# Kernel tuning notes

Hardware: AMD Instinct MI355X
Metric: run time of the kernel (lower is better)

## Reference

```python
import jax, jax.numpy as jnp
import numpy as np
import math

B, NRES, RPR = 1, 384, 3
L = NRES * RPR          # 1152 rigids
CS, CZ = 256, 128
CH, H, PQ, PV = 16, 8, 8, 12


def _ln(x, scale, bias):
    mu = jnp.mean(x, axis=-1, keepdims=True)
    var = jnp.var(x, axis=-1, keepdims=True)
    return (x - mu) * jax.lax.rsqrt(var + 1e-5) * scale + bias


def _quat_to_rot(q):
    q = q / jnp.linalg.norm(q, axis=-1, keepdims=True)
    w, x, y, z = q[..., 0], q[..., 1], q[..., 2], q[..., 3]
    r = jnp.stack([
        1 - 2 * (y * y + z * z), 2 * (x * y - w * z), 2 * (x * z + w * y),
        2 * (x * y + w * z), 1 - 2 * (x * x + z * z), 2 * (y * z - w * x),
        2 * (x * z - w * y), 2 * (y * z + w * x), 1 - 2 * (x * x + y * y),
    ], axis=-1)
    return r.reshape(q.shape[:-1] + (3, 3))


def setup_inputs() -> dict:
    key = jax.random.key(0)
    ks = jax.random.split(key, 20)
    s = jax.random.normal(ks[0], (B, L, CS), jnp.float32)
    z = jax.random.normal(ks[1], (B, NRES, NRES, CZ), jnp.float32)
    rot = _quat_to_rot(jax.random.normal(ks[2], (B, L, 4), jnp.float32))
    trans = 10.0 * jax.random.normal(ks[3], (B, L, 3), jnp.float32)
    mask = jnp.ones((B, L), jnp.float32)
    rigid_to_res_idx = jnp.broadcast_to(jnp.arange(L, dtype=jnp.int32) // RPR, (B, L))
    w = lambda k, sh: 0.02 * jax.random.normal(k, sh, jnp.float32)
    return {
        "s": s, "z": z, "rot": rot, "trans": trans, "mask": mask,
        "ln_s_scale": jnp.ones((CS,), jnp.float32), "ln_s_bias": jnp.zeros((CS,), jnp.float32),
        "ln_z_scale": jnp.ones((CZ,), jnp.float32), "ln_z_bias": jnp.zeros((CZ,), jnp.float32),
        "w_q": w(ks[4], (CS, H * CH)), "w_k": w(ks[5], (CS, H * CH)), "w_v": w(ks[6], (CS, H * CH)),
        "w_qp": w(ks[7], (CS, H * PQ * 3)), "w_kp": w(ks[8], (CS, H * PQ * 3)), "w_vp": w(ks[9], (CS, H * PV * 3)),
        "w_b": w(ks[10], (CZ, H)),
        "head_weights": jnp.full((H,), 0.5413, jnp.float32),  # softplus^-1(1)
        "w_out": w(ks[11], (H * (CH + CZ + PV * 4), CS)),
        "b_out": jnp.zeros((CS,), jnp.float32),
        "rigid_to_res_idx": rigid_to_res_idx,
    }


def reference(s, z, rot, trans, mask, ln_s_scale, ln_s_bias, ln_z_scale, ln_z_bias,
              w_q, w_k, w_v, w_qp, w_kp, w_vp, w_b, head_weights, w_out, b_out,
              rigid_to_res_idx):
    b_, l_ = s.shape[0], s.shape[1]
    idx = rigid_to_res_idx[0]                       # [L] rigid -> residue, shared over batch
    s_ln = _ln(s, ln_s_scale, ln_s_bias)            # [B,L,CS]
    z_ln = _ln(z, ln_z_scale, ln_z_bias)            # [B,N,N,CZ]

    q = (s_ln @ w_q).reshape(b_, l_, H, CH)
    k = (s_ln @ w_k).reshape(b_, l_, H, CH)
    v = (s_ln @ w_v).reshape(b_, l_, H, CH)

    # local points, then rigid-transform to global frame: x_g = R x + t
    q_p = (s_ln @ w_qp).reshape(b_, l_, H, PQ, 3)
    k_p = (s_ln @ w_kp).reshape(b_, l_, H, PQ, 3)
    v_p = (s_ln @ w_vp).reshape(b_, l_, H, PV, 3)
    t5 = trans[:, :, None, None, :]
    q_g = jnp.einsum("blij,blhpj->blhpi", rot, q_p) + t5
    k_g = jnp.einsum("blij,blhpj->blhpi", rot, k_p) + t5
    v_g = jnp.einsum("blij,blhpj->blhpi", rot, v_p) + t5

    # scalar qk term
    a = jnp.einsum("blhc,bjhc->bhlj", q, k) * math.sqrt(1.0 / (3 * CH))
    # pair bias, broadcast residue-pair -> rigid-pair
    b_res = z_ln @ w_b                                # [B,N,N,H]
    b_full = b_res[:, idx][:, :, idx]                 # [B,L,L,H]
    a = a + math.sqrt(1.0 / 3) * jnp.transpose(b_full, (0, 3, 1, 2))
    # point-distance term: ||q-k||^2 = |q|^2 + |k|^2 - 2 q.k (summed over P,3)
    hw = jax.nn.softplus(head_weights) * math.sqrt(1.0 / (3 * (PQ * 9.0 / 2)))
    qq = jnp.sum(q_g * q_g, axis=(-1, -2)).transpose(0, 2, 1)   # [B,H,L]
    kk = jnp.sum(k_g * k_g, axis=(-1, -2)).transpose(0, 2, 1)
    qk = jnp.einsum("blhpc,bjhpc->bhlj", q_g, k_g)
    d2 = qq[:, :, :, None] + kk[:, :, None, :] - 2.0 * qk
    a = a - 0.5 * d2 * hw[None, :, None, None]
    a = a + (mask[:, None, None, :] - 1.0) * 1e9
    attn = jax.nn.softmax(a, axis=-1)                 # [B,H,L,L]

    o = jnp.einsum("bhlj,bjhc->blhc", attn, v)        # [B,L,H,CH]
    o_pt_g = jnp.einsum("bhlj,bjhpc->blhpc", attn, v_g)
    # back to local frame of query rigid: R^T (x - t)
    o_pt = jnp.einsum("blji,blhpj->blhpi", rot, o_pt_g - t5)
    o_pt_norm = jnp.sqrt(jnp.sum(o_pt * o_pt, axis=-1) + 1e-8)  # [B,L,H,PV]
    # pair output: sum attention over rigids belonging to each key residue
    attn_res = attn.reshape(b_, H, l_, NRES, RPR).sum(-1)       # [B,H,L,N]
    z_l = z_ln[:, idx]                                           # [B,L,N,CZ]
    o_pair = jnp.einsum("bhln,blnc->blhc", attn_res, z_l)        # [B,L,H,CZ]

    cat = jnp.concatenate(
        [o, o_pt.reshape(b_, l_, H, PV * 3), o_pt_norm, o_pair], axis=-1
    ).reshape(b_, l_, H * (CH + PV * 4 + CZ))
    return cat @ w_out + b_out                        # [B,L,CS]
```

## Files before the change

kernel.cpp:

```cpp
#include <hip/hip_runtime.h>
#include <hip/hip_bf16.h>

#define L 1152
#define NRES 384
#define CS 256
#define CZ 128
#define H 8
#define CH 16
#define PQ 8
#define PV 12
#define PSTR 1088

#define OFF_SLN  0L
#define OFF_PROJ 294912L
#define OFF_WPK  1548288L
#define OFF_QCAT 1826816L
#define OFF_KCAT 2232320L
#define OFF_VCAT 2637824L
#define OFF_BRES 3227648L
#define OFF_MURS 4407296L
#define OFF_ATTN 4702208L
#define OFF_CAT  15319040L
#define OFF_PAV  18286592L
#define OFF_POP  21825536L
#define OFF_ARES 26544128L
#define OFF_PCAT 30083072L
#define OFF_RST  32442368L

__global__ __launch_bounds__(256) void k_pre(
    const float* wq, const float* wk, const float* wv,
    const float* wqp, const float* wkp, const float* wvp, float* wpack,
    const float* s, const float* lnss, const float* lnsb, float* sln,
    const float* z, const float* lnzs, const float* lnzb,
    const float* wb, float* murs, float* bres_t){
  int bx = blockIdx.x, t = threadIdx.x;
  if(bx < 256){
    int k = bx;
    for(int c=t; c<PSTR; c+=256){
      float v;
      if(c<128)        v = wq [(long)k*128 + c];
      else if(c<256)   v = wk [(long)k*128 + c-128];
      else if(c<384)   v = wv [(long)k*128 + c-256];
      else if(c<576)   v = wqp[(long)k*192 + c-384];
      else if(c<768)   v = wkp[(long)k*192 + c-576];
      else if(c<1056)  v = wvp[(long)k*288 + c-768];
      else             v = 0.f;
      wpack[(long)k*PSTR + c] = v;
    }
    return;
  }
  if(bx < 256 + L){
    int l = bx - 256;
    __shared__ float red[CS];
    float x = s[(long)l*CS + t];
    red[t] = x; __syncthreads();
    for(int st=128; st>0; st>>=1){ if(t<st) red[t]+=red[t+st]; __syncthreads(); }
    float mu = red[0] * (1.f/CS); __syncthreads();
    float d = x - mu;
    red[t] = d*d; __syncthreads();
    for(int st=128; st>0; st>>=1){ if(t<st) red[t]+=red[t+st]; __syncthreads(); }
    float var = red[0]*(1.f/CS);
    sln[(long)l*CS + t] = d*rsqrtf(var + 1e-5f)*lnss[t] + lnsb[t];
    return;
  }
  {
    long rp0 = (long)(bx - 256 - L)*32;
    int r = t>>3, part = t&7;
    long rp = rp0 + r;
    __shared__ __align__(16) float swb[8*132];
    __shared__ float SB[8][2];
    const float4* z4 = (const float4*)z;
    float4 x0 = z4[rp*32 + part*4 + 0];
    float4 x1 = z4[rp*32 + part*4 + 1];
    float4 x2 = z4[rp*32 + part*4 + 2];
    float4 x3 = z4[rp*32 + part*4 + 3];
    #pragma unroll
    for(int k2=0;k2<4;k2++){
      int e = t + k2*256; int h = e>>7, c = e&127;
      swb[h*132 + c] = lnzs[c]*wb[(long)c*8 + h];
    }
    __syncthreads();
    if(t < 64){
      int h = t>>3, seg = t&7;
      float S=0, Bv=0;
      #pragma unroll
      for(int i=0;i<16;i++){
        int c = seg*16+i;
        S  += swb[h*132+c];
        Bv += lnzb[c]*wb[(long)c*8 + h];
      }
      #pragma unroll
      for(int off=1;off<8;off<<=1){ S += __shfl_xor(S,off,64); Bv += __shfl_xor(Bv,off,64); }
      if(seg==0){ SB[h][0]=S; SB[h][1]=Bv; }
    }
    float s1 = x0.x+x0.y+x0.z+x0.w + x1.x+x1.y+x1.z+x1.w
             + x2.x+x2.y+x2.z+x2.w + x3.x+x3.y+x3.z+x3.w;
    float s2 = x0.x*x0.x+x0.y*x0.y+x0.z*x0.z+x0.w*x0.w
             + x1.x*x1.x+x1.y*x1.y+x1.z*x1.z+x1.w*x1.w
             + x2.x*x2.x+x2.y*x2.y+x2.z*x2.z+x2.w*x2.w
             + x3.x*x3.x+x3.y*x3.y+x3.z*x3.z+x3.w*x3.w;
    #pragma unroll
    for(int off=1;off<8;off<<=1){ s1 += __shfl_xor(s1,off,64); s2 += __shfl_xor(s2,off,64); }
    float mu = s1*(1.f/CZ);
    float var = s2*(1.f/CZ) - mu*mu;
    float rstd = rsqrtf(var + 1e-5f);
    if(part==0){ murs[rp*2]=mu; murs[rp*2+1]=rstd; }
    float acc[8];
    const float4* swb4 = (const float4*)swb;
    #pragma unroll
    for(int h=0;h<8;h++){
      float4 wa = swb4[h*33 + part*4 + 0];
      float4 wbv= swb4[h*33 + part*4 + 1];
      float4 wc = swb4[h*33 + part*4 + 2];
      float4 wd = swb4[h*33 + part*4 + 3];
      acc[h] = x0.x*wa.x + x0.y*wa.y + x0.z*wa.z + x0.w*wa.w
             + x1.x*wbv.x+ x1.y*wbv.y+ x1.z*wbv.z+ x1.w*wbv.w
             + x2.x*wc.x + x2.y*wc.y + x2.z*wc.z + x2.w*wc.w
             + x3.x*wd.x + x3.y*wd.y + x3.z*wd.z + x3.w*wd.w;
    }
    #pragma unroll
    for(int off=1;off<8;off<<=1){
      #pragma unroll
      for(int h=0;h<8;h++) acc[h] += __shfl_xor(acc[h],off,64);
    }
    __syncthreads();
    if(part==0){
      #pragma unroll
      for(int h=0;h<8;h++)
        bres_t[(long)h*147456 + rp] = rstd*(acc[h] - mu*SB[h][0]) + SB[h][1];
    }
  }
}

__global__ __launch_bounds__(256) void k_proj(const float* sln, const float* wpack, float* proj){
  int l0 = blockIdx.x*64, c0 = blockIdx.y*64, t = threadIdx.x;
  __shared__ float a_s[32][68];
  __shared__ __align__(16) float w_s[32][68];
  int tr = t>>4, tc = t&15;
  float4 acc[4] = {{0,0,0,0},{0,0,0,0},{0,0,0,0},{0,0,0,0}};
  for(int kc=0; kc<8; kc++){
    int k0 = kc*32;
    {
      int row = t>>2, kk0 = (t&3)*8;
      const float4* src = (const float4*)(sln + (long)(l0+row)*256 + k0 + kk0);
      float4 v0 = src[0], v1 = src[1];
      a_s[kk0+0][row]=v0.x; a_s[kk0+1][row]=v0.y; a_s[kk0+2][row]=v0.z; a_s[kk0+3][row]=v0.w;
      a_s[kk0+4][row]=v1.x; a_s[kk0+5][row]=v1.y; a_s[kk0+6][row]=v1.z; a_s[kk0+7][row]=v1.w;
    }
    #pragma unroll
    for(int kk2=0; kk2<2; kk2++){
      int kk = (t>>4) + 16*kk2;
      *(float4*)&w_s[kk][(t&15)*4] = *(const float4*)(wpack + (long)(k0+kk)*PSTR + c0 + (t&15)*4);
    }
    __syncthreads();
    #pragma unroll 8
    for(int kk=0; kk<32; kk++){
      float4 a4 = *(const float4*)&a_s[kk][tr*4];
      float4 b4 = *(const float4*)&w_s[kk][tc*4];
      acc[0].x+=a4.x*b4.x; acc[0].y+=a4.x*b4.y; acc[0].z+=a4.x*b4.z; acc[0].w+=a4.x*b4.w;
      acc[1].x+=a4.y*b4.x; acc[1].y+=a4.y*b4.y; acc[1].z+=a4.y*b4.z; acc[1].w+=a4.y*b4.w;
      acc[2].x+=a4.z*b4.x; acc[2].y+=a4.z*b4.y; acc[2].z+=a4.z*b4.z; acc[2].w+=a4.z*b4.w;
      acc[3].x+=a4.w*b4.x; acc[3].y+=a4.w*b4.y; acc[3].z+=a4.w*b4.z; acc[3].w+=a4.w*b4.w;
    }
    __syncthreads();
  }
  #pragma unroll
  for(int r=0;r<4;r++)
    *(float4*)(proj + (long)(l0 + tr*4 + r)*PSTR + c0 + tc*4) = acc[r];
}

__global__ __launch_bounds__(256) void k_rigid(const float* proj, const float* rot, const float* trans,
                        const float* mask, const float* hws,
                        float* qcat, float* kcat, float* vcat){
  int l = blockIdx.x, t = threadIdx.x;
  __shared__ float R[9], T[3], hwS[8], qgs[192], kgs[192];
  if(t<9) R[t]=rot[(long)l*9+t];
  if(t<3) T[t]=trans[(long)l*3+t];
  if(t>=16 && t<24) hwS[t-16] = log1pf(expf(hws[t-16]))*0.09622504486493764f;
  __syncthreads();
  const float* pr = proj + (long)l*PSTR;
  if(t<128){
    int h=t>>4, c=t&15;
    qcat[((long)h*44 + c)*L + l] = 0.14433756729740643f * pr[t];
    kcat[((long)h*44 + c)*L + l] = pr[128+t];
    vcat[((long)h*L + l)*64 + c] = pr[256+t];
  }
  if(t < 192){
    int h=t/24, m=t%24, p=m/3, i=m%3;
    float qa = R[i*3+0]*pr[384+h*24+p*3+0] + R[i*3+1]*pr[384+h*24+p*3+1]
             + R[i*3+2]*pr[384+h*24+p*3+2] + T[i];
    float ka = R[i*3+0]*pr[576+h*24+p*3+0] + R[i*3+1]*pr[576+h*24+p*3+1]
             + R[i*3+2]*pr[576+h*24+p*3+2] + T[i];
    qgs[t]=qa; kgs[t]=ka;
    qcat[((long)h*44 + 16 + m)*L + l] = hwS[h]*qa;
    kcat[((long)h*44 + 16 + m)*L + l] = ka;
  }
  for(int it=t; it<288; it+=256){
    int h=it/36, m=it%36, p=m/3, i=m%3;
    float a = R[i*3+0]*pr[768+h*36+p*3+0] + R[i*3+1]*pr[768+h*36+p*3+1]
            + R[i*3+2]*pr[768+h*36+p*3+2] + T[i];
    vcat[((long)h*L + l)*64 + 16 + m] = a;
  }
  if(t < 96){
    int h=t/12, d=t%12;
    vcat[((long)h*L + l)*64 + 52 + d] = 0.f;
  }
  __syncthreads();
  if(t < 8){
    float qq=0, kk=0;
    #pragma unroll
    for(int m=0;m<24;m++){ qq += qgs[t*24+m]*qgs[t*24+m]; kk += kgs[t*24+m]*kgs[t*24+m]; }
    qcat[((long)t*44 + 40)*L + l] = -0.5f*hwS[t]*qq;
    kcat[((long)t*44 + 40)*L + l] = -0.5f*hwS[t]*kk + (mask[l]-1.f)*1e9f;
  }
}

__global__ __launch_bounds__(256) void k_scores(const float* qcat, const float* kcat,
                         const float* bres_t, float* attn){
  int l0 = blockIdx.x*32, j0 = blockIdx.y*128, h = blockIdx.z;
  int t = threadIdx.x;
  __shared__ __align__(16) float q_t[44*36];
  __shared__ __align__(16) float k_t[44*132];
  __shared__ float bp[12*44];
  int rl0 = l0/3, rj0 = j0/3;
  {
    const float* srcq = qcat + (long)h*44*L + l0;
    for(int i=t; i<44*32; i+=256){
      int c = i>>5, ll = i&31;
      q_t[c*36 + ll] = srcq[(long)c*L + ll];
    }
    const float* srck = kcat + (long)h*44*L + j0;
    for(int i=t; i<44*128; i+=256){
      int c = i>>7, jj = i&127;
      k_t[c*132 + jj] = srck[(long)c*L + jj];
    }
    const float* bb = bres_t + (long)h*147456;
    for(int i=t; i<12*44; i+=256){
      int r = i/44, c = i-r*44;
      int rr = rl0+r, cc = rj0+c;
      bp[i] = (rr<NRES && cc<NRES) ? bb[(long)rr*NRES + cc] : 0.f;
    }
  }
  __syncthreads();
  int lg = t>>5, jg = t&31;
  float acc[4][4] = {};
  #pragma unroll 4
  for(int c=0;c<40;c++){
    float4 qv = *(const float4*)&q_t[c*36 + lg*4];
    float4 kv = *(const float4*)&k_t[c*132 + jg*4];
    acc[0][0]+=qv.x*kv.x; acc[0][1]+=qv.x*kv.y; acc[0][2]+=qv.x*kv.z; acc[0][3]+=qv.x*kv.w;
    acc[1][0]+=qv.y*kv.x; acc[1][1]+=qv.y*kv.y; acc[1][2]+=qv.y*kv.z; acc[1][3]+=qv.y*kv.w;
    acc[2][0]+=qv.z*kv.x; acc[2][1]+=qv.z*kv.y; acc[2][2]+=qv.z*kv.z; acc[2][3]+=qv.z*kv.w;
    acc[3][0]+=qv.w*kv.x; acc[3][1]+=qv.w*kv.y; acc[3][2]+=qv.w*kv.z; acc[3][3]+=qv.w*kv.w;
  }
  float4 colc = *(const float4*)&k_t[40*132 + jg*4];
  int jb = j0 + jg*4;
  int rj0i = (jb  )/3 - rj0;
  int rj1i = (jb+1)/3 - rj0;
  int rj2i = (jb+2)/3 - rj0;
  int rj3i = (jb+3)/3 - rj0;
  #pragma unroll
  for(int r=0;r<4;r++){
    int row = lg*4+r;
    float rowc = q_t[40*36 + row];
    const float* bpr = &bp[((l0+row)/3 - rl0)*44];
    float4 o;
    o.x = __expf(acc[r][0] + rowc + colc.x + 0.5773502691896258f*bpr[rj0i]);
    o.y = __expf(acc[r][1] + rowc + colc.y + 0.5773502691896258f*bpr[rj1i]);
    o.z = __expf(acc[r][2] + rowc + colc.z + 0.5773502691896258f*bpr[rj2i]);
    o.w = __expf(acc[r][3] + rowc + colc.w + 0.5773502691896258f*bpr[rj3i]);
    *(float4*)(attn + ((long)h*L + l0+row)*L + jb) = o;
  }
}

__global__ __launch_bounds__(256) void k_rsav(const float* attn, const float* vcat,
                     float* rstat, float* ares, float* pav){
  __shared__ __align__(16) float smem[2*64*68];
  int bx = blockIdx.x, t = threadIdx.x;
  if(bx < 2304){
    float (*es)[1152] = (float(*)[1152])smem;
    long row = (long)bx*4 + (t>>6);
    int lane = t & 63;
    int w = t >> 6;
    const float* p = attn + row*L;
    float v[18];
    float s=0;
    #pragma unroll
    for(int i=0;i<18;i++){ v[i]=p[lane + i*64]; s+=v[i]; }
    #pragma unroll
    for(int off=1;off<64;off<<=1) s+=__shfl_xor(s,off,64);
    float inv = 1.f/s;
    if(lane==0) rstat[row] = inv;
    #pragma unroll
    for(int i=0;i<18;i++) es[w][lane + i*64] = v[i]*inv;
    __syncthreads();
    #pragma unroll
    for(int q=0;q<6;q++){
      int n = lane + q*64;
      ares[row*NRES + n] = es[w][3*n] + es[w][3*n+1] + es[w][3*n+2];
    }
    return;
  }
  int bx2 = bx - 2304;
  int lb = bx2 % 18;
  int rest = bx2 / 18;
  int h = rest & 7, sp = rest >> 3;
  int l0 = lb*64;
  float (*a_s)[68] = (float(*)[68])smem;
  float (*v_s)[68] = (float(*)[68])(smem + 64*68);
  int lgrp = t>>4, dgrp = t&15;
  float4 acc[4] = {{0,0,0,0},{0,0,0,0},{0,0,0,0},{0,0,0,0}};
  const float* abase = attn + ((long)h*L + l0)*L;
  int al = t>>2, jj0s = (t&3)*16;
  for(int jc=sp*3; jc<sp*3+3; jc++){
    int j0 = jc*64;
    {
      const float4* src = (const float4*)(abase + (long)al*L + j0 + jj0s);
      float4 p0 = src[0], p1 = src[1], p2 = src[2], p3 = src[3];
      a_s[jj0s+ 0][al]=p0.x; a_s[jj0s+ 1][al]=p0.y; a_s[jj0s+ 2][al]=p0.z; a_s[jj0s+ 3][al]=p0.w;
      a_s[jj0s+ 4][al]=p1.x; a_s[jj0s+ 5][al]=p1.y; a_s[jj0s+ 6][al]=p1.z; a_s[jj0s+ 7][al]=p1.w;
      a_s[jj0s+ 8][al]=p2.x; a_s[jj0s+ 9][al]=p2.y; a_s[jj0s+10][al]=p2.z; a_s[jj0s+11][al]=p2.w;
      a_s[jj0s+12][al]=p3.x; a_s[jj0s+13][al]=p3.y; a_s[jj0s+14][al]=p3.z; a_s[jj0s+15][al]=p3.w;
    }
    {
      int jj = t>>2, seg = t&3;
      const float4* src = (const float4*)(vcat + ((long)h*L + j0 + jj)*64 + seg*16);
      float4 q0=src[0], q1=src[1], q2=src[2], q3=src[3];
      float4* dst = (float4*)&v_s[jj][seg*16];
      dst[0]=q0; dst[1]=q1; dst[2]=q2; dst[3]=q3;
    }
    __syncthreads();
    #pragma unroll 8
    for(int jj=0; jj<64; jj++){
      float4 av = *(const float4*)&a_s[jj][lgrp*4];
      float4 vv = *(const float4*)&v_s[jj][dgrp*4];
      acc[0].x+=av.x*vv.x; acc[0].y+=av.x*vv.y; acc[0].z+=av.x*vv.z; acc[0].w+=av.x*vv.w;
      acc[1].x+=av.y*vv.x; acc[1].y+=av.y*vv.y; acc[1].z+=av.y*vv.z; acc[1].w+=av.y*vv.w;
      acc[2].x+=av.z*vv.x; acc[2].y+=av.z*vv.y; acc[2].z+=av.z*vv.z; acc[2].w+=av.z*vv.w;
      acc[3].x+=av.w*vv.x; acc[3].y+=av.w*vv.y; acc[3].z+=av.w*vv.z; acc[3].w+=av.w*vv.w;
    }
    __syncthreads();
  }
  #pragma unroll
  for(int r=0;r<4;r++)
    *(float4*)(pav + (((long)sp*H + h)*L + l0 + lgrp*4 + r)*64 + dgrp*4) = acc[r];
}

#define OPAIR_STEP(Z0,Z1,Z2,Z3,NB) { \
    float4 a0 = *(const float4*)&ar[0][th][NB]; \
    float4 a1 = *(const float4*)&ar[1][th][NB]; \
    float4 a2 = *(const float4*)&ar[2][th][NB]; \
    acc[0][0] += a0.x*Z0.x + a0.y*Z1.x + a0.z*Z2.x + a0.w*Z3.x; \
    acc[0][1] += a0.x*Z0.y + a0.y*Z1.y + a0.z*Z2.y + a0.w*Z3.y; \
    acc[0][2] += a0.x*Z0.z + a0.y*Z1.z + a0.z*Z2.z + a0.w*Z3.z; \
    acc[0][3] += a0.x*Z0.w + a0.y*Z1.w + a0.z*Z2.w + a0.w*Z3.w; \
    acc[1][0] += a1.x*Z0.x + a1.y*Z1.x + a1.z*Z2.x + a1.w*Z3.x; \
    acc[1][1] += a1.x*Z0.y + a1.y*Z1.y + a1.z*Z2.y + a1.w*Z3.y; \
    acc[1][2] += a1.x*Z0.z + a1.y*Z1.z + a1.z*Z2.z + a1.w*Z3.z; \
    acc[1][3] += a1.x*Z0.w + a1.y*Z1.w + a1.z*Z2.w + a1.w*Z3.w; \
    acc[2][0] += a2.x*Z0.x + a2.y*Z1.x + a2.z*Z2.x + a2.w*Z3.x; \
    acc[2][1] += a2.x*Z0.y + a2.y*Z1.y + a2.z*Z2.y + a2.w*Z3.y; \
    acc[2][2] += a2.x*Z0.z + a2.y*Z1.z + a2.z*Z2.z + a2.w*Z3.z; \
    acc[2][3] += a2.x*Z0.w + a2.y*Z1.w + a2.z*Z2.w + a2.w*Z3.w; }

__global__ __launch_bounds__(256) void k_oppA(const float* ares, const float* z, const float* murs,
                        const float* sc, const int* ridx, float* po,
                        const float* pav, const float* rstat,
                        const float* rot, const float* trans, float* cat){
  __shared__ __align__(16) float smem[2560];
  int bx = blockIdx.x, t = threadIdx.x;
  if(bx < 1536){
    int r = bx >> 2, sp = bx & 3;
    float (*ar)[H][96] = (float(*)[H][96])smem;
    float* mrs = smem + 2304;
    float* S1s = smem + 2496;
    int rl = ridx[r*3];
    int n0 = sp*96;
    int tc = t&31, th = t>>5;
    const float* zbase = z + ((long)(rl*NRES + n0))*CZ + tc*4;
    float4 zc0 = *(const float4*)(zbase + 0L*CZ);
    float4 zc1 = *(const float4*)(zbase + 1L*CZ);
    float4 zc2 = *(const float4*)(zbase + 2L*CZ);
    float4 zc3 = *(const float4*)(zbase + 3L*CZ);
    for(int i=t;i<192;i+=256) mrs[i]=murs[((long)rl*NRES + n0)*2 + i];
    __syncthreads();
    for(int it=t; it<3*H*96; it+=256){
      int lo = it/(H*96);
      int rem = it - lo*(H*96);
      int h = rem/96, n = rem - h*96;
      ar[lo][h][n] = ares[((long)h*L + r*3+lo)*NRES + n0 + n] * mrs[n*2+1];
    }
    __syncthreads();
    if(t<192){
      int row=t>>3, seg=t&7;
      const float* arr = ((const float*)ar) + row*96 + seg*12;
      const float* mur = mrs + seg*24;
      float s1=0;
      #pragma unroll
      for(int q2=0;q2<12;q2++) s1 += arr[q2]*mur[q2*2];
      s1 += __shfl_xor(s1,1,64); s1 += __shfl_xor(s1,2,64); s1 += __shfl_xor(s1,4,64);
      if(seg==0) S1s[row]=s1;
    }
    __syncthreads();
    float acc[3][4]={};
    for(int nb=0; nb<88; nb+=8){
      float4 zn0 = *(const float4*)(zbase + (long)(nb+4)*CZ);
      float4 zn1 = *(const float4*)(zbase + (long)(nb+5)*CZ);
      float4 zn2 = *(const float4*)(zbase + (long)(nb+6)*CZ);
      float4 zn3 = *(const float4*)(zbase + (long)(nb+7)*CZ);
      OPAIR_STEP(zc0,zc1,zc2,zc3, nb);
      zc0 = *(const float4*)(zbase + (long)(nb+ 8)*CZ);
      zc1 = *(const float4*)(zbase + (long)(nb+ 9)*CZ);
      zc2 = *(const float4*)(zbase + (long)(nb+10)*CZ);
      zc3 = *(const float4*)(zbase + (long)(nb+11)*CZ);
      OPAIR_STEP(zn0,zn1,zn2,zn3, nb+4);
    }
    {
      float4 zn0 = *(const float4*)(zbase + 92L*CZ);
      float4 zn1 = *(const float4*)(zbase + 93L*CZ);
      float4 zn2 = *(const float4*)(zbase + 94L*CZ);
      float4 zn3 = *(const float4*)(zbase + 95L*CZ);
      OPAIR_STEP(zc0,zc1,zc2,zc3, 88);
      OPAIR_STEP(zn0,zn1,zn2,zn3, 92);
    }
    float4 sc4 = *(const float4*)(sc + tc*4);
    #pragma unroll
    for(int lo=0;lo<3;lo++){
      float s1v = S1s[lo*8+th];
      float4 o = { sc4.x*(acc[lo][0]-s1v), sc4.y*(acc[lo][1]-s1v),
                   sc4.z*(acc[lo][2]-s1v), sc4.w*(acc[lo][3]-s1v) };
      *(float4*)(po + ((long)sp*L + (long)(r*3+lo))*1024 + th*128 + tc*4) = o;
    }
    return;
  }
  {
    int bx2 = bx - 1536;
    int lb = bx2 % 36, h = bx2 / 36;
    int l0 = lb*32;
    float (*fin_s)[64] = (float(*)[64])smem;
    #pragma unroll
    for(int k=0;k<2;k++){
      int fi = t + k*256;
      int l = fi>>4, c4 = fi&15;
      long base = (((long)h)*L + l0 + l)*64 + c4*4;
      float4 r = {0,0,0,0};
      #pragma unroll
      for(int p=0;p<6;p++){
        float4 a = *(const float4*)(pav + (long)p*589824 + base);
        r.x+=a.x; r.y+=a.y; r.z+=a.z; r.w+=a.w;
      }
      float inv = rstat[(long)h*L + l0 + l];
      r.x*=inv; r.y*=inv; r.z*=inv; r.w*=inv;
      *(float4*)&fin_s[l][c4*4] = r;
    }
    __syncthreads();
    for(int it=t; it<32*16; it+=256){
      int l=it>>4, c=it&15;
      cat[(long)(l0+l)*1536 + h*192 + c] = fin_s[l][c];
    }
    for(int it=t; it<32*12; it+=256){
      int l=it/12, p=it%12;
      long gl = l0+l;
      float og0 = fin_s[l][16+p*3+0]-trans[gl*3+0];
      float og1 = fin_s[l][16+p*3+1]-trans[gl*3+1];
      float og2 = fin_s[l][16+p*3+2]-trans[gl*3+2];
      float* crow = cat + gl*1536 + h*192;
      float nrm=0;
      #pragma unroll
      for(int i=0;i<3;i++){
        float v = rot[gl*9+0+i]*og0 + rot[gl*9+3+i]*og1 + rot[gl*9+6+i]*og2;
        crow[16+p*3+i]=v; nrm+=v*v;
      }
      crow[52+p]=sqrtf(nrm+1e-8f);
    }
  }
}

__global__ __launch_bounds__(256) void k_postB(const float* po, const float* bi, float* cat){
  int i = blockIdx.x*256 + threadIdx.x;
  const float4* p = (const float4*)po;
  float4 a = p[i], b = p[i + 294912], c = p[i + 589824], d = p[i + 884736];
  int l = i>>8, rem = i&255;
  int h = rem>>5, c4 = rem&31;
  float4 bv = ((const float4*)bi)[c4];
  float4 r = {a.x+b.x+c.x+d.x+bv.x, a.y+b.y+c.y+d.y+bv.y,
              a.z+b.z+c.z+d.z+bv.z, a.w+b.w+c.w+d.w+bv.w};
  ((float4*)cat)[(long)l*384 + h*48 + 16 + c4] = r;
}

__global__ __launch_bounds__(256) void k_final(const float* cat, const float* wout, float* pcat){
  int l0 = blockIdx.x*64, c0 = blockIdx.y*64, kp = blockIdx.z, t = threadIdx.x;
  __shared__ __align__(16) float a_s[64][68];
  __shared__ __align__(16) float w_s[64][68];
  int lgrp = t>>4, cgrp = t&15;
  float4 acc[4] = {{0,0,0,0},{0,0,0,0},{0,0,0,0},{0,0,0,0}};
  int al = t>>2, ks0 = (t&3)*16;
  for(int kc=0; kc<3; kc++){
    int k0 = kp*192 + kc*64;
    {
      const float4* src = (const float4*)(cat + (long)(l0+al)*1536 + k0 + ks0);
      float4 p0 = src[0], p1 = src[1], p2 = src[2], p3 = src[3];
      a_s[ks0+ 0][al]=p0.x; a_s[ks0+ 1][al]=p0.y; a_s[ks0+ 2][al]=p0.z; a_s[ks0+ 3][al]=p0.w;
      a_s[ks0+ 4][al]=p1.x; a_s[ks0+ 5][al]=p1.y; a_s[ks0+ 6][al]=p1.z; a_s[ks0+ 7][al]=p1.w;
      a_s[ks0+ 8][al]=p2.x; a_s[ks0+ 9][al]=p2.y; a_s[ks0+10][al]=p2.z; a_s[ks0+11][al]=p2.w;
      a_s[ks0+12][al]=p3.x; a_s[ks0+13][al]=p3.y; a_s[ks0+14][al]=p3.z; a_s[ks0+15][al]=p3.w;
    }
    {
      int kk = t>>2, seg = t&3;
      const float4* src = (const float4*)(wout + (long)(k0+kk)*256 + c0 + seg*16);
      float4 q0=src[0], q1=src[1], q2=src[2], q3=src[3];
      float4* dst = (float4*)&w_s[kk][seg*16];
      dst[0]=q0; dst[1]=q1; dst[2]=q2; dst[3]=q3;
    }
    __syncthreads();
    #pragma unroll 8
    for(int kk=0; kk<64; kk++){
      float4 av = *(const float4*)&a_s[kk][lgrp*4];
      float4 wv = *(const float4*)&w_s[kk][cgrp*4];
      acc[0].x+=av.x*wv.x; acc[0].y+=av.x*wv.y; acc[0].z+=av.x*wv.z; acc[0].w+=av.x*wv.w;
      acc[1].x+=av.y*wv.x; acc[1].y+=av.y*wv.y; acc[1].z+=av.y*wv.z; acc[1].w+=av.y*wv.w;
      acc[2].x+=av.z*wv.x; acc[2].y+=av.z*wv.y; acc[2].z+=av.z*wv.z; acc[2].w+=av.z*wv.w;
      acc[3].x+=av.w*wv.x; acc[3].y+=av.w*wv.y; acc[3].z+=av.w*wv.z; acc[3].w+=av.w*wv.w;
    }
    __syncthreads();
  }
  #pragma unroll
  for(int r=0;r<4;r++)
    *(float4*)(pcat + ((long)kp*L + l0 + lgrp*4 + r)*256 + c0 + cgrp*4) = acc[r];
}

__global__ __launch_bounds__(256) void k_redout(const float* pcat, const float* bout, float* out){
  int i = blockIdx.x*256 + threadIdx.x;
  const float4* p = (const float4*)pcat;
  float4 bv = ((const float4*)bout)[i&63];
  float4 r = bv;
  #pragma unroll
  for(int p8=0;p8<8;p8++){
    float4 a = p[i + (long)p8*73728];
    r.x+=a.x; r.y+=a.y; r.z+=a.z; r.w+=a.w;
  }
  ((float4*)out)[i] = r;
}

extern "C" void kernel_launch(void* const* d_in, const int* in_sizes, int n_in,
                              void* d_out, int out_size, void* d_ws, size_t ws_size,
                              hipStream_t stream) {
  const float* s      = (const float*)d_in[0];
  const float* z      = (const float*)d_in[1];
  const float* rot    = (const float*)d_in[2];
  const float* trans  = (const float*)d_in[3];
  const float* mask   = (const float*)d_in[4];
  const float* lnss   = (const float*)d_in[5];
  const float* lnsb   = (const float*)d_in[6];
  const float* lnzs   = (const float*)d_in[7];
  const float* lnzb   = (const float*)d_in[8];
  const float* wq     = (const float*)d_in[9];
  const float* wk     = (const float*)d_in[10];
  const float* wv     = (const float*)d_in[11];
  const float* wqp    = (const float*)d_in[12];
  const float* wkp    = (const float*)d_in[13];
  const float* wvp    = (const float*)d_in[14];
  const float* wb     = (const float*)d_in[15];
  const float* hws    = (const float*)d_in[16];
  const float* wout   = (const float*)d_in[17];
  const float* bout   = (const float*)d_in[18];
  const int*  ridx    = (const int*)d_in[19];

  float* ws  = (float*)d_ws;
  float* out = (float*)d_out;

  float* sln  = ws + OFF_SLN;
  float* proj = ws + OFF_PROJ;
  float* wpk  = ws + OFF_WPK;
  float* qcat = ws + OFF_QCAT;
  float* kcat = ws + OFF_KCAT;
  float* vcat = ws + OFF_VCAT;
  float* bres = ws + OFF_BRES;
  float* murs = ws + OFF_MURS;
  float* attn = ws + OFF_ATTN;
  float* cat  = ws + OFF_CAT;
  float* pcat = ws + OFF_PCAT;
  float* pav  = ws + OFF_PAV;
  float* po   = ws + OFF_POP;
  float* ares = ws + OFF_ARES;
  float* rst  = ws + OFF_RST;

  k_pre<<<dim3(256 + L + NRES*NRES/32), dim3(256), 0, stream>>>(
      wq, wk, wv, wqp, wkp, wvp, wpk,
      s, lnss, lnsb, sln,
      z, lnzs, lnzb, wb, murs, bres);
  k_proj<<<dim3(18,17), dim3(256), 0, stream>>>(sln, wpk, proj);
  k_rigid<<<dim3(L), dim3(256), 0, stream>>>(proj, rot, trans, mask, hws, qcat, kcat, vcat);
  k_scores<<<dim3(L/32, L/128, H), dim3(256), 0, stream>>>(qcat, kcat, bres, attn);
  k_rsav<<<dim3(2304 + 864), dim3(256), 0, stream>>>(attn, vcat, rst, ares, pav);
  k_oppA<<<dim3(1536 + 288), dim3(256), 0, stream>>>(ares, z, murs, lnzs, ridx, po,
                                                     pav, rst, rot, trans, cat);
  k_postB<<<dim3(1152), dim3(256), 0, stream>>>(po, lnzb, cat);
  k_final<<<dim3(L/64, 4, 8), dim3(256), 0, stream>>>(cat, wout, pcat);
  k_redout<<<dim3(288), dim3(256), 0, stream>>>(pcat, bout, out);
}
```

Before: 295.3 us.

## Halve pair-output split count and fuse partial-sum reduction into output GEMM

The pair-output kernel now splits each residue's key range into two 192-wide chunks instead of four 96-wide ones, so it writes two partial buffers rather than four. The separate k_postB kernel, which summed the partials, added the bias and wrote into the concat buffer, is removed. The final GEMM now loads the pair columns straight from the two partial buffers, adding them and the bias while staging into shared memory. This drops one launch and a round trip through the concat buffer, at the cost of fewer blocks and more shared memory per block in k_oppA.

```diff
diff --git a/kernel.cpp b/kernel.cpp
--- a/kernel.cpp
+++ b/kernel.cpp
@@ -367,43 +367,44 @@
                         const float* sc, const int* ridx, float* po,
                         const float* pav, const float* rstat,
                         const float* rot, const float* trans, float* cat){
-  __shared__ __align__(16) float smem[2560];
+  __shared__ __align__(16) float smem[5016];
   int bx = blockIdx.x, t = threadIdx.x;
-  if(bx < 1536){
-    int r = bx >> 2, sp = bx & 3;
-    float (*ar)[H][96] = (float(*)[H][96])smem;
-    float* mrs = smem + 2304;
-    float* S1s = smem + 2496;
+  if(bx < 768){
+    int r = bx >> 1, sp = bx & 1;
+    float (*ar)[H][192] = (float(*)[H][192])smem;
+    float* mrs = smem + 4608 - 4608 + 4608;
+    mrs = smem + 4608;
+    float* S1s = smem + 4992;
     int rl = ridx[r*3];
-    int n0 = sp*96;
+    int n0 = sp*192;
     int tc = t&31, th = t>>5;
     const float* zbase = z + ((long)(rl*NRES + n0))*CZ + tc*4;
     float4 zc0 = *(const float4*)(zbase + 0L*CZ);
     float4 zc1 = *(const float4*)(zbase + 1L*CZ);
     float4 zc2 = *(const float4*)(zbase + 2L*CZ);
     float4 zc3 = *(const float4*)(zbase + 3L*CZ);
-    for(int i=t;i<192;i+=256) mrs[i]=murs[((long)rl*NRES + n0)*2 + i];
-    __syncthreads();
-    for(int it=t; it<3*H*96; it+=256){
-      int lo = it/(H*96);
-      int rem = it - lo*(H*96);
-      int h = rem/96, n = rem - h*96;
+    for(int i=t;i<384;i+=256) mrs[i]=murs[((long)rl*NRES + n0)*2 + i];
+    __syncthreads();
+    for(int it=t; it<3*H*192; it+=256){
+      int lo = it/(H*192);
+      int rem = it - lo*(H*192);
+      int h = rem/192, n = rem - h*192;
       ar[lo][h][n] = ares[((long)h*L + r*3+lo)*NRES + n0 + n] * mrs[n*2+1];
     }
     __syncthreads();
     if(t<192){
       int row=t>>3, seg=t&7;
-      const float* arr = ((const float*)ar) + row*96 + seg*12;
-      const float* mur = mrs + seg*24;
+      const float* arr = ((const float*)ar) + row*192 + seg*24;
+      const float* mur = mrs + seg*48;
       float s1=0;
       #pragma unroll
-      for(int q2=0;q2<12;q2++) s1 += arr[q2]*mur[q2*2];
+      for(int q2=0;q2<24;q2++) s1 += arr[q2]*mur[q2*2];
       s1 += __shfl_xor(s1,1,64); s1 += __shfl_xor(s1,2,64); s1 += __shfl_xor(s1,4,64);
       if(seg==0) S1s[row]=s1;
     }
     __syncthreads();
     float acc[3][4]={};
-    for(int nb=0; nb<88; nb+=8){
+    for(int nb=0; nb<184; nb+=8){
       float4 zn0 = *(const float4*)(zbase + (long)(nb+4)*CZ);
       float4 zn1 = *(const float4*)(zbase + (long)(nb+5)*CZ);
       float4 zn2 = *(const float4*)(zbase + (long)(nb+6)*CZ);
@@ -416,12 +417,12 @@
       OPAIR_STEP(zn0,zn1,zn2,zn3, nb+4);
     }
     {
-      float4 zn0 = *(const float4*)(zbase + 92L*CZ);
-      float4 zn1 = *(const float4*)(zbase + 93L*CZ);
-      float4 zn2 = *(const float4*)(zbase + 94L*CZ);
-      float4 zn3 = *(const float4*)(zbase + 95L*CZ);
-      OPAIR_STEP(zc0,zc1,zc2,zc3, 88);
-      OPAIR_STEP(zn0,zn1,zn2,zn3, 92);
+      float4 zn0 = *(const float4*)(zbase + 188L*CZ);
+      float4 zn1 = *(const float4*)(zbase + 189L*CZ);
+      float4 zn2 = *(const float4*)(zbase + 190L*CZ);
+      float4 zn3 = *(const float4*)(zbase + 191L*CZ);
+      OPAIR_STEP(zc0,zc1,zc2,zc3, 184);
+      OPAIR_STEP(zn0,zn1,zn2,zn3, 188);
     }
     float4 sc4 = *(const float4*)(sc + tc*4);
     #pragma unroll
@@ -434,7 +435,7 @@
     return;
   }
   {
-    int bx2 = bx - 1536;
+    int bx2 = bx - 768;
     int lb = bx2 % 36, h = bx2 / 36;
     int l0 = lb*32;
     float (*fin_s)[64] = (float(*)[64])smem;
@@ -476,19 +477,8 @@
   }
 }
 
-__global__ __launch_bounds__(256) void k_postB(const float* po, const float* bi, float* cat){
-  int i = blockIdx.x*256 + threadIdx.x;
-  const float4* p = (const float4*)po;
-  float4 a = p[i], b = p[i + 294912], c = p[i + 589824], d = p[i + 884736];
-  int l = i>>8, rem = i&255;
-  int h = rem>>5, c4 = rem&31;
-  float4 bv = ((const float4*)bi)[c4];
-  float4 r = {a.x+b.x+c.x+d.x+bv.x, a.y+b.y+c.y+d.y+bv.y,
-              a.z+b.z+c.z+d.z+bv.z, a.w+b.w+c.w+d.w+bv.w};
-  ((float4*)cat)[(long)l*384 + h*48 + 16 + c4] = r;
-}
-
-__global__ __launch_bounds__(256) void k_final(const float* cat, const float* wout, float* pcat){
+__global__ __launch_bounds__(256) void k_final(const float* cat, const float* po,
+                        const float* bi, const float* wout, float* pcat){
   int l0 = blockIdx.x*64, c0 = blockIdx.y*64, kp = blockIdx.z, t = threadIdx.x;
   __shared__ __align__(16) float a_s[64][68];
   __shared__ __align__(16) float w_s[64][68];
@@ -497,13 +487,27 @@
   int al = t>>2, ks0 = (t&3)*16;
   for(int kc=0; kc<3; kc++){
     int k0 = kp*192 + kc*64;
-    {
+    if(kc==0){
       const float4* src = (const float4*)(cat + (long)(l0+al)*1536 + k0 + ks0);
       float4 p0 = src[0], p1 = src[1], p2 = src[2], p3 = src[3];
       a_s[ks0+ 0][al]=p0.x; a_s[ks0+ 1][al]=p0.y; a_s[ks0+ 2][al]=p0.z; a_s[ks0+ 3][al]=p0.w;
       a_s[ks0+ 4][al]=p1.x; a_s[ks0+ 5][al]=p1.y; a_s[ks0+ 6][al]=p1.z; a_s[ks0+ 7][al]=p1.w;
       a_s[ks0+ 8][al]=p2.x; a_s[ks0+ 9][al]=p2.y; a_s[ks0+10][al]=p2.z; a_s[ks0+11][al]=p2.w;
       a_s[ks0+12][al]=p3.x; a_s[ks0+13][al]=p3.y; a_s[ks0+14][al]=p3.z; a_s[ks0+15][al]=p3.w;
+    } else {
+      int m = (kc-1)*64 + ks0;
+      long pb = (long)(l0+al)*1024 + kp*128 + m;
+      const float4* s0 = (const float4*)(po + pb);
+      const float4* s1 = (const float4*)(po + 1179648L + pb);
+      const float4* bb = (const float4*)(bi + m);
+      #pragma unroll
+      for(int q=0;q<4;q++){
+        float4 a = s0[q], b = s1[q], bv = bb[q];
+        a_s[ks0+q*4+0][al]=a.x+b.x+bv.x;
+        a_s[ks0+q*4+1][al]=a.y+b.y+bv.y;
+        a_s[ks0+q*4+2][al]=a.z+b.z+bv.z;
+        a_s[ks0+q*4+3][al]=a.w+b.w+bv.w;
+      }
     }
     {
       int kk = t>>2, seg = t&3;
@@ -593,9 +597,8 @@
   k_rigid<<<dim3(L), dim3(256), 0, stream>>>(proj, rot, trans, mask, hws, qcat, kcat, vcat);
   k_scores<<<dim3(L/32, L/128, H), dim3(256), 0, stream>>>(qcat, kcat, bres, attn);
   k_rsav<<<dim3(2304 + 864), dim3(256), 0, stream>>>(attn, vcat, rst, ares, pav);
-  k_oppA<<<dim3(1536 + 288), dim3(256), 0, stream>>>(ares, z, murs, lnzs, ridx, po,
-                                                     pav, rst, rot, trans, cat);
-  k_postB<<<dim3(1152), dim3(256), 0, stream>>>(po, lnzb, cat);
-  k_final<<<dim3(L/64, 4, 8), dim3(256), 0, stream>>>(cat, wout, pcat);
+  k_oppA<<<dim3(768 + 288), dim3(256), 0, stream>>>(ares, z, murs, lnzs, ridx, po,
+                                                    pav, rst, rot, trans, cat);
+  k_final<<<dim3(L/64, 4, 8), dim3(256), 0, stream>>>(cat, po, lnzb, wout, pcat);
   k_redout<<<dim3(288), dim3(256), 0, stream>>>(pcat, bout, out);
 }
```

Result: slower. 301.8 us (+2.2%).
